# Kernel optimization log

Hardware: AMD Instinct MI355X
Metric: run time of the kernel (lower is better)

The kernel has to match this reference:

```python
import jax
import jax.numpy as jnp
import numpy as np

H, W = 224, 224
N = 1024  # batch_size(128) * num_batches(8) total masked samples per stream
EPS = 1e-10  # sum_of_weights_initial_value


def setup_inputs() -> dict:
    key = jax.random.key(0)
    k = jax.random.split(key, 6)
    masks_a = jax.random.uniform(k[0], (N, H, W), dtype=jnp.float32)
    # binary_mask_generator produces {0,1} masks
    masks_b = (jax.random.uniform(k[1], (N, H, W)) > 0.5).astype(jnp.float32)
    sims = jax.random.uniform(k[2], (N,), dtype=jnp.float32)
    sims_texture = jax.random.uniform(k[3], (N,), dtype=jnp.float32)
    sims_color = jax.random.uniform(k[4], (N,), dtype=jnp.float32)
    sims_shape = jax.random.uniform(k[5], (N,), dtype=jnp.float32)
    return {
        "masks_a": masks_a,
        "sims": sims,
        "masks_b": masks_b,
        "sims_texture": sims_texture,
        "sims_color": sims_color,
        "sims_shape": sims_shape,
    }


def _relax_importance(masks_a, sims, masks_b, sims_texture, sims_color, sims_shape):
    """Sequential per-sample online weighted mean over the pixel plane.

    importance_{i} = importance_{i-1} + m_i * (s_i - importance_{i-1}) / sw_i,
    sw_i = sw_{i-1} + m_i.  Texture/color/shape streams share masks_b (and thus
    have identical sum_of_weights trajectories), exactly as in the source.
    """
    zeros = jnp.zeros((H, W), jnp.float32)
    sw0 = jnp.full((H, W), EPS, jnp.float32)

    def step(carry, xs):
        sw_a, imp, sw_b, imp_t, imp_c, imp_s = carry
        ma, sa, mb, st, sc, ss = xs
        sw_a = sw_a + ma
        imp = imp + ma * (sa - imp) / sw_a
        sw_b = sw_b + mb
        inv = mb / sw_b
        imp_t = imp_t + inv * (st - imp_t)
        imp_c = imp_c + inv * (sc - imp_c)
        imp_s = imp_s + inv * (ss - imp_s)
        return (sw_a, imp, sw_b, imp_t, imp_c, imp_s), None

    init = (sw0, zeros, sw0, zeros, zeros, zeros)
    (sw_a, imp, sw_b, imp_t, imp_c, imp_s), _ = jax.lax.scan(
        step, init, (masks_a, sims, masks_b, sims_texture, sims_color, sims_shape)
    )

    def norm(x):  # torch .std() uses ddof=1
        return (x - x.mean()) / jnp.std(x, ddof=1)

    return jnp.stack([norm(imp), norm(imp_t), norm(imp_c), norm(imp_s)])  # [4,H,W]


def reference(masks_a, sims, masks_b, sims_texture, sims_color, sims_shape):
    return _relax_importance(masks_a, sims, masks_b, sims_texture, sims_color, sims_shape)
```

## Files before the change

### kernel.cpp

```cpp
#include <hip/hip_runtime.h>
#include <math.h>

#define HW (224 * 224)
#define HW4 (HW / 4)
#define NSAMP 1024
#define NCHUNK 16
#define CHUNK (NSAMP / NCHUNK)
#define EPSW 1e-10f

__device__ __forceinline__ void fma4(float4& acc, const float4 m, const float s) {
  acc.x = fmaf(m.x, s, acc.x);
  acc.y = fmaf(m.y, s, acc.y);
  acc.z = fmaf(m.z, s, acc.z);
  acc.w = fmaf(m.w, s, acc.w);
}
__device__ __forceinline__ void add4(float4& acc, const float4 m) {
  acc.x += m.x; acc.y += m.y; acc.z += m.z; acc.w += m.w;
}

__global__ __launch_bounds__(256) void relax_partial(
    const float4* __restrict__ A4, const float4* __restrict__ B4,
    const float* __restrict__ sa, const float* __restrict__ st,
    const float* __restrict__ sc, const float* __restrict__ ss,
    float* __restrict__ part) {
  __shared__ float4 s4[CHUNK];
  const int tid = threadIdx.x;
  const int i0 = blockIdx.y * CHUNK;
  if (tid < CHUNK)
    s4[tid] = make_float4(sa[i0 + tid], st[i0 + tid], sc[i0 + tid], ss[i0 + tid]);
  __syncthreads();

  const int q = blockIdx.x * 256 + tid;
  const float4* ap = A4 + (size_t)i0 * HW4 + q;
  const float4* bp = B4 + (size_t)i0 * HW4 + q;

  float4 Wa = {0,0,0,0}, Sa = {0,0,0,0}, Wb = {0,0,0,0};
  float4 St = {0,0,0,0}, Sc = {0,0,0,0}, Ss = {0,0,0,0};
#pragma unroll 4
  for (int j = 0; j < CHUNK; ++j) {
    const float4 ma = ap[(size_t)j * HW4];
    const float4 mb = bp[(size_t)j * HW4];
    const float4 sv = s4[j];
    add4(Wa, ma);
    fma4(Sa, ma, sv.x);
    add4(Wb, mb);
    fma4(St, mb, sv.y);
    fma4(Sc, mb, sv.z);
    fma4(Ss, mb, sv.w);
  }
  const int p = 4 * q;
  float* w;
  w = &part[0 * HW + p];
  atomicAdd(w + 0, Wa.x); atomicAdd(w + 1, Wa.y); atomicAdd(w + 2, Wa.z); atomicAdd(w + 3, Wa.w);
  w = &part[1 * HW + p];
  atomicAdd(w + 0, Sa.x); atomicAdd(w + 1, Sa.y); atomicAdd(w + 2, Sa.z); atomicAdd(w + 3, Sa.w);
  w = &part[2 * HW + p];
  atomicAdd(w + 0, Wb.x); atomicAdd(w + 1, Wb.y); atomicAdd(w + 2, Wb.z); atomicAdd(w + 3, Wb.w);
  w = &part[3 * HW + p];
  atomicAdd(w + 0, St.x); atomicAdd(w + 1, St.y); atomicAdd(w + 2, St.z); atomicAdd(w + 3, St.w);
  w = &part[4 * HW + p];
  atomicAdd(w + 0, Sc.x); atomicAdd(w + 1, Sc.y); atomicAdd(w + 2, Sc.z); atomicAdd(w + 3, Sc.w);
  w = &part[5 * HW + p];
  atomicAdd(w + 0, Ss.x); atomicAdd(w + 1, Ss.y); atomicAdd(w + 2, Ss.z); atomicAdd(w + 3, Ss.w);
}

__global__ __launch_bounds__(256) void relax_stats(
    const float4* __restrict__ part4, double* __restrict__ stats) {
  const int q = blockIdx.x * 256 + threadIdx.x;
  const float4 Wa = part4[0 * HW4 + q], Sa = part4[1 * HW4 + q];
  const float4 Wb = part4[2 * HW4 + q];
  const float4 St = part4[3 * HW4 + q], Sc = part4[4 * HW4 + q], Ss = part4[5 * HW4 + q];

  double v[8] = {0, 0, 0, 0, 0, 0, 0, 0};
  const float* wa = &Wa.x; const float* sa = &Sa.x; const float* wb = &Wb.x;
  const float* st = &St.x; const float* sc = &Sc.x; const float* ss = &Ss.x;
#pragma unroll
  for (int k = 0; k < 4; ++k) {
    const float x0 = sa[k] / (EPSW + wa[k]);
    const float invb = 1.0f / (EPSW + wb[k]);
    const float x1 = st[k] * invb, x2 = sc[k] * invb, x3 = ss[k] * invb;
    v[0] += x0; v[1] += (double)x0 * x0;
    v[2] += x1; v[3] += (double)x1 * x1;
    v[4] += x2; v[5] += (double)x2 * x2;
    v[6] += x3; v[7] += (double)x3 * x3;
  }

#pragma unroll
  for (int k = 0; k < 8; ++k)
#pragma unroll
    for (int off = 32; off; off >>= 1)
      v[k] += __shfl_down(v[k], off);

  if ((threadIdx.x & 63) == 0) {
#pragma unroll
    for (int k = 0; k < 8; ++k) atomicAdd(&stats[k], v[k]);
  }
}

__global__ __launch_bounds__(256) void relax_norm(
    const float4* __restrict__ part4, const double* __restrict__ stats,
    float4* __restrict__ out4) {
  const int q = blockIdx.x * 256 + threadIdx.x;
  const int m = blockIdx.y;

  float4 x;
  if (m == 0) {
    const float4 W = part4[0 * HW4 + q], S = part4[1 * HW4 + q];
    x = make_float4(S.x / (EPSW + W.x), S.y / (EPSW + W.y),
                    S.z / (EPSW + W.z), S.w / (EPSW + W.w));
  } else {
    const float4 W = part4[2 * HW4 + q], S = part4[(2 + m) * HW4 + q];
    x = make_float4(S.x / (EPSW + W.x), S.y / (EPSW + W.y),
                    S.z / (EPSW + W.z), S.w / (EPSW + W.w));
  }
  const double sum = stats[2 * m], sumsq = stats[2 * m + 1];
  const double mean = sum / (double)HW;
  const double var = (sumsq - sum * sum / (double)HW) / (double)(HW - 1);
  const float istd = (float)(1.0 / sqrt(var));
  const float fm = (float)mean;
  out4[m * HW4 + q] = make_float4((x.x - fm) * istd, (x.y - fm) * istd,
                                  (x.z - fm) * istd, (x.w - fm) * istd);
}

extern "C" void kernel_launch(void* const* d_in, const int* in_sizes, int n_in,
                              void* d_out, int out_size, void* d_ws, size_t ws_size,
                              hipStream_t stream) {
  const float4* A4 = (const float4*)d_in[0];
  const float* sa  = (const float*)d_in[1];
  const float4* B4 = (const float4*)d_in[2];
  const float* st  = (const float*)d_in[3];
  const float* sc  = (const float*)d_in[4];
  const float* ss  = (const float*)d_in[5];
  float4* out4 = (float4*)d_out;

  double* stats = (double*)d_ws;
  float* part = (float*)((char*)d_ws + 64);

  hipMemsetAsync(d_ws, 0, 64 + (size_t)6 * HW * sizeof(float), stream);

  dim3 g1(HW4 / 256, NCHUNK);
  relax_partial<<<g1, 256, 0, stream>>>(A4, (const float4*)B4, sa, st, sc, ss, part);
  relax_stats<<<dim3(HW4 / 256), 256, 0, stream>>>((const float4*)part, stats);
  relax_norm<<<dim3(HW4 / 256, 4), 256, 0, stream>>>((const float4*)part, stats, out4);
}
```

Before: 164.7 us.

## Replace atomic partial accumulation with per-chunk buffers and a reduce pass

The partial-sum kernel now writes each chunk's six per-pixel accumulators to its own workspace slice, and a separate reduce kernel sums them. This removes the float atomics and the large memset, but only when the workspace is big enough; otherwise it falls back to the old atomic path. The chunk count doubles to 32 for more parallelism, and the inner loop is explicitly double-buffered so loads are issued ahead. The reduce kernel also computes the stats and writes the final per-pixel means to a map, so the norm kernel no longer recomputes the divisions. The cost is extra workspace traffic (32×6 planes written and re-read).

```diff
diff --git a/kernel.cpp b/kernel.cpp
--- a/kernel.cpp
+++ b/kernel.cpp
@@ -4,9 +4,10 @@
 #define HW (224 * 224)
 #define HW4 (HW / 4)
 #define NSAMP 1024
-#define NCHUNK 16
+#define NCHUNK 32
 #define CHUNK (NSAMP / NCHUNK)
 #define EPSW 1e-10f
+#define PXBLK (HW4 / 256)
 
 __device__ __forceinline__ void fma4(float4& acc, const float4 m, const float s) {
   acc.x = fmaf(m.x, s, acc.x);
@@ -17,12 +18,77 @@
 __device__ __forceinline__ void add4(float4& acc, const float4 m) {
   acc.x += m.x; acc.y += m.y; acc.z += m.z; acc.w += m.w;
 }
+__device__ __forceinline__ void accstat(const float4 x, double& s, double& s2) {
+  s  += (double)x.x + (double)x.y + (double)x.z + (double)x.w;
+  s2 += (double)x.x * x.x + (double)x.y * x.y + (double)x.z * x.z + (double)x.w * x.w;
+}
+
+struct Acc6 { float4 Wa, Sa, Wb, St, Sc, Ss; };
+
+__device__ __forceinline__ Acc6 chunk_accumulate(
+    const float4* __restrict__ ap, const float4* __restrict__ bp,
+    const float4* __restrict__ s4) {
+  Acc6 r;
+  r.Wa = r.Sa = r.Wb = r.St = r.Sc = r.Ss = make_float4(0, 0, 0, 0);
+
+  float4 abuf[2][4], bbuf[2][4];
+#pragma unroll
+  for (int k = 0; k < 4; ++k) {
+    abuf[0][k] = ap[(size_t)k * HW4];
+    bbuf[0][k] = bp[(size_t)k * HW4];
+  }
+#pragma unroll
+  for (int g = 0; g < CHUNK / 4; ++g) {
+    const int cur = g & 1;
+    if (g + 1 < CHUNK / 4) {
+#pragma unroll
+      for (int k = 0; k < 4; ++k) {
+        abuf[cur ^ 1][k] = ap[(size_t)((g + 1) * 4 + k) * HW4];
+        bbuf[cur ^ 1][k] = bp[(size_t)((g + 1) * 4 + k) * HW4];
+      }
+    }
+#pragma unroll
+    for (int k = 0; k < 4; ++k) {
+      const float4 ma = abuf[cur][k], mb = bbuf[cur][k];
+      const float4 sv = s4[g * 4 + k];
+      add4(r.Wa, ma);
+      fma4(r.Sa, ma, sv.x);
+      add4(r.Wb, mb);
+      fma4(r.St, mb, sv.y);
+      fma4(r.Sc, mb, sv.z);
+      fma4(r.Ss, mb, sv.w);
+    }
+  }
+  return r;
+}
 
 __global__ __launch_bounds__(256) void relax_partial(
     const float4* __restrict__ A4, const float4* __restrict__ B4,
     const float* __restrict__ sa, const float* __restrict__ st,
     const float* __restrict__ sc, const float* __restrict__ ss,
-    float* __restrict__ part) {
+    float4* __restrict__ part) {
+  __shared__ float4 s4[CHUNK];
+  const int tid = threadIdx.x;
+  const int c = blockIdx.y;
+  const int i0 = c * CHUNK;
+  if (tid < CHUNK)
+    s4[tid] = make_float4(sa[i0 + tid], st[i0 + tid], sc[i0 + tid], ss[i0 + tid]);
+  __syncthreads();
+
+  const int q = blockIdx.x * 256 + tid;
+  const Acc6 r = chunk_accumulate(A4 + (size_t)i0 * HW4 + q,
+                                  B4 + (size_t)i0 * HW4 + q, s4);
+
+  float4* w = part + (size_t)c * 6 * HW4 + q;
+  w[0 * HW4] = r.Wa; w[1 * HW4] = r.Sa; w[2 * HW4] = r.Wb;
+  w[3 * HW4] = r.St; w[4 * HW4] = r.Sc; w[5 * HW4] = r.Ss;
+}
+
+__global__ __launch_bounds__(256) void relax_partial_atomic(
+    const float4* __restrict__ A4, const float4* __restrict__ B4,
+    const float* __restrict__ sa, const float* __restrict__ st,
+    const float* __restrict__ sc, const float* __restrict__ ss,
+    float* __restrict__ part6) {
   __shared__ float4 s4[CHUNK];
   const int tid = threadIdx.x;
   const int i0 = blockIdx.y * CHUNK;
@@ -31,88 +97,90 @@
   __syncthreads();
 
   const int q = blockIdx.x * 256 + tid;
-  const float4* ap = A4 + (size_t)i0 * HW4 + q;
-  const float4* bp = B4 + (size_t)i0 * HW4 + q;
-
-  float4 Wa = {0,0,0,0}, Sa = {0,0,0,0}, Wb = {0,0,0,0};
-  float4 St = {0,0,0,0}, Sc = {0,0,0,0}, Ss = {0,0,0,0};
-#pragma unroll 4
-  for (int j = 0; j < CHUNK; ++j) {
-    const float4 ma = ap[(size_t)j * HW4];
-    const float4 mb = bp[(size_t)j * HW4];
-    const float4 sv = s4[j];
-    add4(Wa, ma);
-    fma4(Sa, ma, sv.x);
-    add4(Wb, mb);
-    fma4(St, mb, sv.y);
-    fma4(Sc, mb, sv.z);
-    fma4(Ss, mb, sv.w);
-  }
+  const Acc6 r = chunk_accumulate(A4 + (size_t)i0 * HW4 + q,
+                                  B4 + (size_t)i0 * HW4 + q, s4);
   const int p = 4 * q;
+  const float* v;
   float* w;
-  w = &part[0 * HW + p];
-  atomicAdd(w + 0, Wa.x); atomicAdd(w + 1, Wa.y); atomicAdd(w + 2, Wa.z); atomicAdd(w + 3, Wa.w);
-  w = &part[1 * HW + p];
-  atomicAdd(w + 0, Sa.x); atomicAdd(w + 1, Sa.y); atomicAdd(w + 2, Sa.z); atomicAdd(w + 3, Sa.w);
-  w = &part[2 * HW + p];
-  atomicAdd(w + 0, Wb.x); atomicAdd(w + 1, Wb.y); atomicAdd(w + 2, Wb.z); atomicAdd(w + 3, Wb.w);
-  w = &part[3 * HW + p];
-  atomicAdd(w + 0, St.x); atomicAdd(w + 1, St.y); atomicAdd(w + 2, St.z); atomicAdd(w + 3, St.w);
-  w = &part[4 * HW + p];
-  atomicAdd(w + 0, Sc.x); atomicAdd(w + 1, Sc.y); atomicAdd(w + 2, Sc.z); atomicAdd(w + 3, Sc.w);
-  w = &part[5 * HW + p];
-  atomicAdd(w + 0, Ss.x); atomicAdd(w + 1, Ss.y); atomicAdd(w + 2, Ss.z); atomicAdd(w + 3, Ss.w);
-}
-
-__global__ __launch_bounds__(256) void relax_stats(
-    const float4* __restrict__ part4, double* __restrict__ stats) {
-  const int q = blockIdx.x * 256 + threadIdx.x;
-  const float4 Wa = part4[0 * HW4 + q], Sa = part4[1 * HW4 + q];
-  const float4 Wb = part4[2 * HW4 + q];
-  const float4 St = part4[3 * HW4 + q], Sc = part4[4 * HW4 + q], Ss = part4[5 * HW4 + q];
+  w = &part6[0 * HW + p]; v = &r.Wa.x;
+  atomicAdd(w, v[0]); atomicAdd(w + 1, v[1]); atomicAdd(w + 2, v[2]); atomicAdd(w + 3, v[3]);
+  w = &part6[1 * HW + p]; v = &r.Sa.x;
+  atomicAdd(w, v[0]); atomicAdd(w + 1, v[1]); atomicAdd(w + 2, v[2]); atomicAdd(w + 3, v[3]);
+  w = &part6[2 * HW + p]; v = &r.Wb.x;
+  atomicAdd(w, v[0]); atomicAdd(w + 1, v[1]); atomicAdd(w + 2, v[2]); atomicAdd(w + 3, v[3]);
+  w = &part6[3 * HW + p]; v = &r.St.x;
+  atomicAdd(w, v[0]); atomicAdd(w + 1, v[1]); atomicAdd(w + 2, v[2]); atomicAdd(w + 3, v[3]);
+  w = &part6[4 * HW + p]; v = &r.Sc.x;
+  atomicAdd(w, v[0]); atomicAdd(w + 1, v[1]); atomicAdd(w + 2, v[2]); atomicAdd(w + 3, v[3]);
+  w = &part6[5 * HW + p]; v = &r.Ss.x;
+  atomicAdd(w, v[0]); atomicAdd(w + 1, v[1]); atomicAdd(w + 2, v[2]); atomicAdd(w + 3, v[3]);
+}
+
+__device__ __forceinline__ void finish_pixel(
+    const float4 Wa, const float4 Sa, const float4 Wb,
+    const float4 St, const float4 Sc, const float4 Ss,
+    int q, float4* __restrict__ xmap, double* __restrict__ stats) {
+  const float4 x0 = make_float4(Sa.x / (EPSW + Wa.x), Sa.y / (EPSW + Wa.y),
+                                Sa.z / (EPSW + Wa.z), Sa.w / (EPSW + Wa.w));
+  const float4 inv = make_float4(1.f / (EPSW + Wb.x), 1.f / (EPSW + Wb.y),
+                                 1.f / (EPSW + Wb.z), 1.f / (EPSW + Wb.w));
+  const float4 x1 = make_float4(St.x * inv.x, St.y * inv.y, St.z * inv.z, St.w * inv.w);
+  const float4 x2 = make_float4(Sc.x * inv.x, Sc.y * inv.y, Sc.z * inv.z, Sc.w * inv.w);
+  const float4 x3 = make_float4(Ss.x * inv.x, Ss.y * inv.y, Ss.z * inv.z, Ss.w * inv.w);
+
+  xmap[0 * HW4 + q] = x0;
+  xmap[1 * HW4 + q] = x1;
+  xmap[2 * HW4 + q] = x2;
+  xmap[3 * HW4 + q] = x3;
 
   double v[8] = {0, 0, 0, 0, 0, 0, 0, 0};
-  const float* wa = &Wa.x; const float* sa = &Sa.x; const float* wb = &Wb.x;
-  const float* st = &St.x; const float* sc = &Sc.x; const float* ss = &Ss.x;
-#pragma unroll
-  for (int k = 0; k < 4; ++k) {
-    const float x0 = sa[k] / (EPSW + wa[k]);
-    const float invb = 1.0f / (EPSW + wb[k]);
-    const float x1 = st[k] * invb, x2 = sc[k] * invb, x3 = ss[k] * invb;
-    v[0] += x0; v[1] += (double)x0 * x0;
-    v[2] += x1; v[3] += (double)x1 * x1;
-    v[4] += x2; v[5] += (double)x2 * x2;
-    v[6] += x3; v[7] += (double)x3 * x3;
-  }
-
+  accstat(x0, v[0], v[1]);
+  accstat(x1, v[2], v[3]);
+  accstat(x2, v[4], v[5]);
+  accstat(x3, v[6], v[7]);
 #pragma unroll
   for (int k = 0; k < 8; ++k)
 #pragma unroll
     for (int off = 32; off; off >>= 1)
       v[k] += __shfl_down(v[k], off);
-
   if ((threadIdx.x & 63) == 0) {
 #pragma unroll
     for (int k = 0; k < 8; ++k) atomicAdd(&stats[k], v[k]);
   }
 }
 
+__global__ __launch_bounds__(256) void relax_reduce(
+    const float4* __restrict__ part, float4* __restrict__ xmap,
+    double* __restrict__ stats) {
+  const int q = blockIdx.x * 256 + threadIdx.x;
+  float4 a0 = {0,0,0,0}, a1 = {0,0,0,0}, a2 = {0,0,0,0};
+  float4 a3 = {0,0,0,0}, a4 = {0,0,0,0}, a5 = {0,0,0,0};
+#pragma unroll 4
+  for (int c = 0; c < NCHUNK; ++c) {
+    const float4* w = part + (size_t)c * 6 * HW4 + q;
+    const float4 t0 = w[0 * HW4], t1 = w[1 * HW4], t2 = w[2 * HW4];
+    const float4 t3 = w[3 * HW4], t4 = w[4 * HW4], t5 = w[5 * HW4];
+    add4(a0, t0); add4(a1, t1); add4(a2, t2);
+    add4(a3, t3); add4(a4, t4); add4(a5, t5);
+  }
+  finish_pixel(a0, a1, a2, a3, a4, a5, q, xmap, stats);
+}
+
+__global__ __launch_bounds__(256) void relax_reduce_atomicpath(
+    const float4* __restrict__ part6, float4* __restrict__ xmap,
+    double* __restrict__ stats) {
+  const int q = blockIdx.x * 256 + threadIdx.x;
+  finish_pixel(part6[0 * HW4 + q], part6[1 * HW4 + q], part6[2 * HW4 + q],
+               part6[3 * HW4 + q], part6[4 * HW4 + q], part6[5 * HW4 + q],
+               q, xmap, stats);
+}
+
 __global__ __launch_bounds__(256) void relax_norm(
-    const float4* __restrict__ part4, const double* __restrict__ stats,
+    const float4* __restrict__ xmap, const double* __restrict__ stats,
     float4* __restrict__ out4) {
   const int q = blockIdx.x * 256 + threadIdx.x;
   const int m = blockIdx.y;
-
-  float4 x;
-  if (m == 0) {
-    const float4 W = part4[0 * HW4 + q], S = part4[1 * HW4 + q];
-    x = make_float4(S.x / (EPSW + W.x), S.y / (EPSW + W.y),
-                    S.z / (EPSW + W.z), S.w / (EPSW + W.w));
-  } else {
-    const float4 W = part4[2 * HW4 + q], S = part4[(2 + m) * HW4 + q];
-    x = make_float4(S.x / (EPSW + W.x), S.y / (EPSW + W.y),
-                    S.z / (EPSW + W.z), S.w / (EPSW + W.w));
-  }
+  const float4 x = xmap[m * HW4 + q];
   const double sum = stats[2 * m], sumsq = stats[2 * m + 1];
   const double mean = sum / (double)HW;
   const double var = (sumsq - sum * sum / (double)HW) / (double)(HW - 1);
@@ -134,12 +202,22 @@
   float4* out4 = (float4*)d_out;
 
   double* stats = (double*)d_ws;
-  float* part = (float*)((char*)d_ws + 64);
-
-  hipMemsetAsync(d_ws, 0, 64 + (size_t)6 * HW * sizeof(float), stream);
-
-  dim3 g1(HW4 / 256, NCHUNK);
-  relax_partial<<<g1, 256, 0, stream>>>(A4, (const float4*)B4, sa, st, sc, ss, part);
-  relax_stats<<<dim3(HW4 / 256), 256, 0, stream>>>((const float4*)part, stats);
-  relax_norm<<<dim3(HW4 / 256, 4), 256, 0, stream>>>((const float4*)part, stats, out4);
-}
+  float4* xmap = (float4*)((char*)d_ws + 64);
+  char* rest = (char*)d_ws + 64 + (size_t)4 * HW * sizeof(float);
+  const size_t need_main =
+      64 + (size_t)4 * HW * sizeof(float) + (size_t)NCHUNK * 6 * HW * sizeof(float);
+
+  hipMemsetAsync(d_ws, 0, 64, stream);
+
+  if (ws_size >= need_main) {
+    float4* part = (float4*)rest;
+    relax_partial<<<dim3(PXBLK, NCHUNK), 256, 0, stream>>>(A4, B4, sa, st, sc, ss, part);
+    relax_reduce<<<dim3(PXBLK), 256, 0, stream>>>(part, xmap, stats);
+  } else {
+    float* part6 = (float*)rest;
+    hipMemsetAsync(part6, 0, (size_t)6 * HW * sizeof(float), stream);
+    relax_partial_atomic<<<dim3(PXBLK, NCHUNK), 256, 0, stream>>>(A4, B4, sa, st, sc, ss, part6);
+    relax_reduce_atomicpath<<<dim3(PXBLK), 256, 0, stream>>>((const float4*)part6, xmap, stats);
+  }
+  relax_norm<<<dim3(PXBLK, 4), 256, 0, stream>>>(xmap, stats, out4);
+}
```

Measured after the change: 149.2 us. -9.4%, faster.
